# Kernel tuning notes

Measured on AMD Instinct MI355X. Metric: run time of the kernel, lower is better.

Reference implementation:

```python
import jax, jax.numpy as jnp
import numpy as np

EPS = 1e-6
BASE_TAU = 1.0  # temperature, learnable_tau=False


def setup_inputs() -> dict:
    key = jax.random.key(0)
    k1, k2, k3 = jax.random.split(key, 3)
    n, b, t, h = 16, 4, 2048, 1024
    num_blocks = 24
    return {
        "values": jax.random.normal(k1, (n, b, t, h), dtype=jnp.float32),
        "w_query": jax.random.normal(k2, (num_blocks, h), dtype=jnp.float32) * 0.02,
        "key_pos_bias": jax.random.normal(k3, (num_blocks, h), dtype=jnp.float32) * 0.02,
        "position": 16,
    }


def reference(values, w_query, key_pos_bias, position):
    # values: [n, b, t, h] stacked completed block outputs, n == position
    fp = values.astype(jnp.float32)
    # weight-free RMSNorm (BlockAttnRes._rms_norm)
    inv = jax.lax.rsqrt(jnp.mean(fp * fp, axis=-1, keepdims=True) + EPS)
    keys = fp * inv
    # positional bias for the first `position` block slots
    keys = keys + key_pos_bias[:position].astype(keys.dtype)[:, None, None, :]
    query = w_query[position].astype(jnp.float32)  # [h]
    scale = jnp.sqrt(jnp.float32(values.shape[-1])) * BASE_TAU
    scores = jnp.einsum('h,nbth->nbt', query, keys) / scale  # [n, b, t]
    alpha = jax.nn.softmax(scores, axis=0)                    # softmax over history n
    routed = jnp.einsum('nbt,nbth->bth', alpha, fp).astype(values.dtype)
    alpha_bth = jnp.transpose(alpha, (1, 2, 0))               # [b, t, n]
    return routed, alpha_bth
```

## Files before the change

### kernel.cpp

```cpp
#include <hip/hip_runtime.h>
#include <math.h>

#define H     1024
#define NBLK  16
#define BT    8192
#define ROUTED_SIZE (BT * H)
#define SCALE_INV (1.0f / 32.0f)

__global__ __launch_bounds__(1024) void qb_kernel(
    const float* __restrict__ w_query,
    const float* __restrict__ key_pos_bias,
    const int*   __restrict__ pos_p,
    float*       __restrict__ qb)
{
    const int n    = threadIdx.x >> 6;
    const int lane = threadIdx.x & 63;
    const int pos  = *pos_p;

    const float* q = w_query      + (size_t)pos * H;
    const float* b = key_pos_bias + (size_t)n   * H;

    float s = 0.0f;
#pragma unroll
    for (int j = 0; j < 4; ++j) {
        const int h = lane * 16 + j * 4;
        const float4 qv = *(const float4*)(q + h);
        const float4 bv = *(const float4*)(b + h);
        s += qv.x * bv.x + qv.y * bv.y + qv.z * bv.z + qv.w * bv.w;
    }
#pragma unroll
    for (int off = 32; off; off >>= 1) s += __shfl_xor(s, off, 64);
    if (lane == 0) qb[n] = s;
}

__global__ __launch_bounds__(256, 4) void block_attn_res_kernel(
    const float* __restrict__ values,
    const float* __restrict__ w_query,
    const int*   __restrict__ pos_p,
    const float* __restrict__ qb,
    float*       __restrict__ out)
{
    const int bt   = blockIdx.x;
    const int tid  = threadIdx.x;
    const int lane = tid & 63;
    const int wave = tid >> 6;
    const int h0   = tid << 2;

    const int pos = *pos_p;
    const float4 q = *(const float4*)(w_query + (size_t)pos * H + h0);

    float4 v[NBLK];
    const float* vbase = values + (size_t)bt * H + h0;
#pragma unroll
    for (int n = 0; n < NBLK; ++n)
        v[n] = *(const float4*)(vbase + (size_t)n * (size_t)BT * H);

    __shared__ float red[2][NBLK][4];

#pragma unroll
    for (int n = 0; n < NBLK; ++n) {
        float ss = v[n].x * v[n].x + v[n].y * v[n].y
                 + v[n].z * v[n].z + v[n].w * v[n].w;
        float qv = q.x * v[n].x + q.y * v[n].y
                 + q.z * v[n].z + q.w * v[n].w;
#pragma unroll
        for (int off = 32; off; off >>= 1) {
            ss += __shfl_xor(ss, off, 64);
            qv += __shfl_xor(qv, off, 64);
        }
        if (lane == 0) { red[0][n][wave] = ss; red[1][n][wave] = qv; }
    }
    __syncthreads();

    float score[NBLK];
    float m = -3.402823466e38f;
#pragma unroll
    for (int n = 0; n < NBLK; ++n) {
        const float SS = red[0][n][0] + red[0][n][1] + red[0][n][2] + red[0][n][3];
        const float QV = red[1][n][0] + red[1][n][1] + red[1][n][2] + red[1][n][3];
        const float inv = rsqrtf(SS * (1.0f / (float)H) + 1e-6f);
        score[n] = (inv * QV + qb[n]) * SCALE_INV;
        m = fmaxf(m, score[n]);
    }
    float sum = 0.0f;
#pragma unroll
    for (int n = 0; n < NBLK; ++n) {
        score[n] = __expf(score[n] - m);
        sum += score[n];
    }
    const float rs = 1.0f / sum;

    float4 acc = make_float4(0.f, 0.f, 0.f, 0.f);
#pragma unroll
    for (int n = 0; n < NBLK; ++n) {
        const float a = score[n] * rs;
        acc.x += a * v[n].x;  acc.y += a * v[n].y;
        acc.z += a * v[n].z;  acc.w += a * v[n].w;
    }
    *(float4*)(out + (size_t)bt * H + h0) = acc;

    if (tid < NBLK)
        out[(size_t)ROUTED_SIZE + (size_t)bt * NBLK + tid] = score[tid] * rs;
}

extern "C" void kernel_launch(void* const* d_in, const int* in_sizes, int n_in,
                              void* d_out, int out_size, void* d_ws, size_t ws_size,
                              hipStream_t stream) {
    const float* values       = (const float*)d_in[0];
    const float* w_query      = (const float*)d_in[1];
    const float* key_pos_bias = (const float*)d_in[2];
    const int*   position     = (const int*)d_in[3];
    float*       out          = (float*)d_out;
    float*       qb           = (float*)d_ws;

    hipLaunchKernelGGL(qb_kernel, dim3(1), dim3(1024), 0, stream,
                       w_query, key_pos_bias, position, qb);
    hipLaunchKernelGGL(block_attn_res_kernel, dim3(BT), dim3(256), 0, stream,
                       values, w_query, position, qb, out);
}
```

Measured before the change: 702.6 us.

## Restructure score reduction through shared memory and use nontemporal loads/stores

```diff
diff --git a/kernel.cpp b/kernel.cpp
--- a/kernel.cpp
+++ b/kernel.cpp
@@ -6,6 +6,8 @@
 #define BT    8192
 #define ROUTED_SIZE (BT * H)
 #define SCALE_INV (1.0f / 32.0f)
+
+typedef float v4f __attribute__((ext_vector_type(4)));
 
 __global__ __launch_bounds__(1024) void qb_kernel(
     const float* __restrict__ w_query,
@@ -40,67 +42,71 @@
     const float* __restrict__ qb,
     float*       __restrict__ out)
 {
-    const int bt   = blockIdx.x;
-    const int tid  = threadIdx.x;
-    const int lane = tid & 63;
-    const int wave = tid >> 6;
-    const int h0   = tid << 2;
+    const int bt  = blockIdx.x;
+    const int tid = threadIdx.x;
+    const int h0  = tid << 2;
 
     const int pos = *pos_p;
-    const float4 q = *(const float4*)(w_query + (size_t)pos * H + h0);
+    const v4f q = *(const v4f*)(w_query + (size_t)pos * H + h0);
 
-    float4 v[NBLK];
+    v4f v[NBLK];
     const float* vbase = values + (size_t)bt * H + h0;
 #pragma unroll
     for (int n = 0; n < NBLK; ++n)
-        v[n] = *(const float4*)(vbase + (size_t)n * (size_t)BT * H);
+        v[n] = __builtin_nontemporal_load((const v4f*)(vbase + (size_t)n * BT * H));
 
-    __shared__ float red[2][NBLK][4];
+    __shared__ float2 pv[NBLK][256];
 
 #pragma unroll
     for (int n = 0; n < NBLK; ++n) {
-        float ss = v[n].x * v[n].x + v[n].y * v[n].y
-                 + v[n].z * v[n].z + v[n].w * v[n].w;
-        float qv = q.x * v[n].x + q.y * v[n].y
-                 + q.z * v[n].z + q.w * v[n].w;
+        const v4f x  = v[n];
+        const v4f xx = x * x;
+        const v4f qx = q * x;
+        const float ss = (xx[0] + xx[1]) + (xx[2] + xx[3]);
+        const float qv = (qx[0] + qx[1]) + (qx[2] + qx[3]);
+        pv[n][tid] = make_float2(ss, qv);
+    }
+    __syncthreads();
+
+    {
+        const int n2 = tid >> 4;
+        const int c  = tid & 15;
+        float ss = 0.0f, qv = 0.0f;
 #pragma unroll
-        for (int off = 32; off; off >>= 1) {
+        for (int k = 0; k < 16; ++k) {
+            const float2 p = pv[n2][k * 16 + c];
+            ss += p.x; qv += p.y;
+        }
+#pragma unroll
+        for (int off = 1; off <= 8; off <<= 1) {
             ss += __shfl_xor(ss, off, 64);
             qv += __shfl_xor(qv, off, 64);
         }
-        if (lane == 0) { red[0][n][wave] = ss; red[1][n][wave] = qv; }
+        if (c == 0) {
+            const float inv = rsqrtf(ss * (1.0f / (float)H) + 1e-6f);
+            pv[n2][0].x = (inv * qv + qb[n2]) * SCALE_INV;
+        }
     }
     __syncthreads();
 
-    float score[NBLK];
     float m = -3.402823466e38f;
 #pragma unroll
-    for (int n = 0; n < NBLK; ++n) {
-        const float SS = red[0][n][0] + red[0][n][1] + red[0][n][2] + red[0][n][3];
-        const float QV = red[1][n][0] + red[1][n][1] + red[1][n][2] + red[1][n][3];
-        const float inv = rsqrtf(SS * (1.0f / (float)H) + 1e-6f);
-        score[n] = (inv * QV + qb[n]) * SCALE_INV;
-        m = fmaxf(m, score[n]);
-    }
+    for (int n = 0; n < NBLK; ++n) m = fmaxf(m, pv[n][0].x);
+
+    float a[NBLK];
     float sum = 0.0f;
 #pragma unroll
-    for (int n = 0; n < NBLK; ++n) {
-        score[n] = __expf(score[n] - m);
-        sum += score[n];
-    }
+    for (int n = 0; n < NBLK; ++n) { a[n] = __expf(pv[n][0].x - m); sum += a[n]; }
     const float rs = 1.0f / sum;
 
-    float4 acc = make_float4(0.f, 0.f, 0.f, 0.f);
+    v4f acc = {0.0f, 0.0f, 0.0f, 0.0f};
 #pragma unroll
-    for (int n = 0; n < NBLK; ++n) {
-        const float a = score[n] * rs;
-        acc.x += a * v[n].x;  acc.y += a * v[n].y;
-        acc.z += a * v[n].z;  acc.w += a * v[n].w;
-    }
-    *(float4*)(out + (size_t)bt * H + h0) = acc;
+    for (int n = 0; n < NBLK; ++n) acc += (a[n] * rs) * v[n];
+    __builtin_nontemporal_store(acc, (v4f*)(out + (size_t)bt * H + h0));
 
     if (tid < NBLK)
-        out[(size_t)ROUTED_SIZE + (size_t)bt * NBLK + tid] = score[tid] * rs;
+        out[(size_t)ROUTED_SIZE + (size_t)bt * NBLK + tid]
+            = __expf(pv[tid][0].x - m) * rs;
 }
 
 extern "C" void kernel_launch(void* const* d_in, const int* in_sizes, int n_in,
```

New measurement: 674.0 us. 4.1% less time.
